# Optimization experiments

Measured on AMD Instinct MI355X. Metric: run time of the kernel, lower is better.

## Reference

```python
import jax, jax.numpy as jnp
import numpy as np

EPS = 1e-08
LN_EPS = 1e-05


def _layernorm(x, g, b):
    mu = jnp.mean(x, axis=-1, keepdims=True)
    var = jnp.var(x, axis=-1, keepdims=True)
    return (x - mu) * jax.lax.rsqrt(var + LN_EPS) * g + b


def _prob(x):
    x = jnp.tanh(x) * 0.499 + 0.5
    return jnp.clip(x / (jnp.sum(x, axis=-1, keepdims=True) + EPS), EPS)


def setup_inputs() -> dict:
    key = jax.random.key(0)
    ks = jax.random.split(key, 8)
    B, N, D = 8, 2048, 1024
    H = 4 * D
    s = 0.02
    return {
        'q': jax.random.normal(ks[0], (B, N, D), jnp.float32),
        'k': jax.random.normal(ks[1], (B, N, D), jnp.float32),
        'v': jax.random.normal(ks[2], (B, N, D), jnp.float32),
        'W_diff': jax.random.normal(ks[3], (D, D), jnp.float32) * s,
        'b_diff': jnp.zeros((D,), jnp.float32),
        'ln_g': jnp.ones((D,), jnp.float32),
        'ln_b': jnp.zeros((D,), jnp.float32),
        'W1': jax.random.normal(ks[4], (H, D), jnp.float32) * s,
        'b1': jnp.zeros((H,), jnp.float32),
        'W2': jax.random.normal(ks[5], (D, H), jnp.float32) * s,
        'b2': jnp.zeros((D,), jnp.float32),
    }


def reference(q, k, v, W_diff, b_diff, ln_g, ln_b, W1, b1, W2, b2):
    D = q.shape[-1]
    q_prob = _prob(q)  # [B,N,D]
    k_prob = _prob(k)  # [B,N,D]
    log_ratio = jnp.log(q_prob) - jnp.log(k_prob)  # [B,N,D]
    # sid[b,i,j] = sum_d (q_prob[b,i,d] - k_prob[b,i,d]) * log_ratio[b,j,d]
    sid = jnp.einsum('bnd,bmd->bnm', q_prob - k_prob, log_ratio)
    sid_sim = -sid
    attn = jax.nn.softmax(sid_sim / (D ** 0.5), axis=-1)  # [B,N,N]
    attn_feat = jnp.einsum('bnm,bmd->bnd', attn, v)
    f_diff = (v - attn_feat) @ W_diff.T + b_diff + q
    h = _layernorm(f_diff, ln_g, ln_b)
    mlp = jax.nn.gelu(h @ W1.T + b1, approximate=False) @ W2.T + b2
    out = mlp + f_diff
    return _layernorm(out, ln_g, ln_b)
```

## Files before the change

kernel.cpp:

```cpp
#include <hip/hip_runtime.h>
#include <math.h>

typedef unsigned short u16;
typedef __attribute__((ext_vector_type(4))) unsigned short u16x4;
typedef __attribute__((ext_vector_type(8))) short s16x8;
typedef __attribute__((ext_vector_type(4))) float f32x4;
typedef __attribute__((ext_vector_type(4))) float f4v;

#define DEVI static __device__ __forceinline__

DEVI u16 f2bf(float f) {
  union { float f; unsigned u; } c; c.f = f;
  return (u16)((c.u + 0x7FFFu + ((c.u >> 16) & 1u)) >> 16);
}
DEVI float bf2f(u16 h) {
  union { unsigned u; float f; } c; c.u = ((unsigned)h) << 16;
  return c.f;
}
DEVI unsigned cvt_pk_bf16(float lo, float hi) {
  unsigned r;
  asm("v_cvt_pk_bf16_f32 %0, %1, %2" : "=v"(r) : "v"(lo), "v"(hi));
  return r;
}

DEVI float tanh_fast(float x) {
  float e = __expf(2.0f * x);
  float r = __builtin_amdgcn_rcpf(e + 1.0f);
  return fmaf(-2.0f, r, 1.0f);
}
DEVI float gelu_fast(float x) {
  float x2 = x * x;
  float u = x * fmaf(x2, 0.0356774081f, 0.7978845608f);
  float e = __expf(2.0f * u);
  float r = __builtin_amdgcn_rcpf(e + 1.0f);
  float t = fmaf(-2.0f, r, 1.0f);
  float hx = 0.5f * x;
  return fmaf(hx, t, hx);
}

DEVI void load_lds16(const void* g, void* l) {
  __builtin_amdgcn_global_load_lds(
      (const __attribute__((address_space(1))) void*)g,
      (__attribute__((address_space(3))) void*)l, 16, 0, 0);
}

#define BAR_VM6() asm volatile("s_waitcnt vmcnt(6)\n\ts_barrier" ::: "memory")
#define BAR_VM4() asm volatile("s_waitcnt vmcnt(4)\n\ts_barrier" ::: "memory")
#define BAR_VM2() asm volatile("s_waitcnt vmcnt(2)\n\ts_barrier" ::: "memory")
#define BAR_VM0() asm volatile("s_waitcnt vmcnt(0)\n\ts_barrier" ::: "memory")
#define BAR_PLAIN() asm volatile("s_barrier" ::: "memory")


__global__ __launch_bounds__(256) void cast_bf4_kernel(
    const float* __restrict__ in, u16* __restrict__ out, int n4) {
  int i = blockIdx.x * 256 + threadIdx.x;
  if (i >= n4) return;
  f4v f = ((const f4v*)in)[i];
  u16x4 o;
  o[0] = f2bf(f[0]); o[1] = f2bf(f[1]); o[2] = f2bf(f[2]); o[3] = f2bf(f[3]);
  ((u16x4*)out)[i] = o;
}

__global__ __launch_bounds__(256) void prob_kernel(
    const float* __restrict__ q, const float* __restrict__ k,
    u16* __restrict__ A, u16* __restrict__ Bm) {
  const int D = 1024;
  size_t row = blockIdx.x;
  int t = threadIdx.x;
  f4v qv = ((const f4v*)(q + row * D))[t];
  f4v kv = ((const f4v*)(k + row * D))[t];
  float tq[4], tk[4];
  float sq = 0.f, sk = 0.f;
#pragma unroll
  for (int i = 0; i < 4; i++) {
    tq[i] = tanh_fast(qv[i]) * 0.499f + 0.5f;
    tk[i] = tanh_fast(kv[i]) * 0.499f + 0.5f;
    sq += tq[i]; sk += tk[i];
  }
#pragma unroll
  for (int off = 32; off > 0; off >>= 1) {
    sq += __shfl_xor(sq, off);
    sk += __shfl_xor(sk, off);
  }
  __shared__ float sbq[4], sbk[4];
  int lane = t & 63, w = t >> 6;
  if (lane == 0) { sbq[w] = sq; sbk[w] = sk; }
  __syncthreads();
  sq = sbq[0] + sbq[1] + sbq[2] + sbq[3];
  sk = sbk[0] + sbk[1] + sbk[2] + sbk[3];
  float iq = 1.0f / (sq + 1e-8f), ik = 1.0f / (sk + 1e-8f);
  u16x4 av, bv;
#pragma unroll
  for (int i = 0; i < 4; i++) {
    float qp = fmaxf(tq[i] * iq, 1e-8f);
    float kp = fmaxf(tk[i] * ik, 1e-8f);
    av[i] = f2bf(qp - kp);
    bv[i] = f2bf(__logf(qp) - __logf(kp));
  }
  ((u16x4*)(A + row * D))[t] = av;
  ((u16x4*)(Bm + row * D))[t] = bv;
}

__global__ __launch_bounds__(256) void transpose_v_kernel(
    const float* __restrict__ v, u16* __restrict__ Vt) {
  const int N = 2048, D = 1024;
  __shared__ float tile[32][33];
  int b = blockIdx.z;
  int d0 = blockIdx.x * 32, n0 = blockIdx.y * 32;
  int tx = threadIdx.x & 31, ty = threadIdx.x >> 5;
  const float* vb = v + (size_t)b * N * D;
  u16* vtb = Vt + (size_t)b * N * D;
#pragma unroll
  for (int i = 0; i < 4; i++)
    tile[ty + i * 8][tx] = vb[(size_t)(n0 + ty + i * 8) * D + d0 + tx];
  __syncthreads();
#pragma unroll
  for (int i = 0; i < 4; i++)
    vtb[(size_t)(d0 + ty + i * 8) * N + n0 + tx] = f2bf(tile[tx][ty + i * 8]);
}

__global__ __launch_bounds__(256) void softmax_rows_kernel(u16* __restrict__ S) {
  const int NN = 2048;
  size_t row = blockIdx.x;
  u16* r = S + row * NN;
  int t = threadIdx.x;
  s16x8 vv = ((const s16x8*)r)[t];
  float x[8];
  float mx = -1e30f;
#pragma unroll
  for (int i = 0; i < 8; i++) { x[i] = bf2f((u16)vv[i]); mx = fmaxf(mx, x[i]); }
#pragma unroll
  for (int off = 32; off > 0; off >>= 1) mx = fmaxf(mx, __shfl_xor(mx, off));
  __shared__ float sm[4], ss[4];
  int lane = t & 63, w = t >> 6;
  if (lane == 0) sm[w] = mx;
  __syncthreads();
  mx = fmaxf(fmaxf(sm[0], sm[1]), fmaxf(sm[2], sm[3]));
  float sum = 0.f;
#pragma unroll
  for (int i = 0; i < 8; i++) { x[i] = __expf(x[i] - mx); sum += x[i]; }
#pragma unroll
  for (int off = 32; off > 0; off >>= 1) sum += __shfl_xor(sum, off);
  if (lane == 0) ss[w] = sum;
  __syncthreads();
  float inv = 1.0f / (ss[0] + ss[1] + ss[2] + ss[3]);
  s16x8 ov;
#pragma unroll
  for (int i = 0; i < 8; i++) ov[i] = (short)f2bf(x[i] * inv);
  ((s16x8*)r)[t] = ov;
}

template <int OUT_BF16>
__global__ __launch_bounds__(256) void layernorm_rows_kernel(
    const float* __restrict__ in, void* __restrict__ outp,
    const float* __restrict__ g, const float* __restrict__ bia) {
  const int D = 1024;
  size_t row = blockIdx.x;
  int t = threadIdx.x;
  f4v xv = ((const f4v*)(in + row * D))[t];
  float s = xv[0] + xv[1] + xv[2] + xv[3];
  float s2 = xv[0] * xv[0] + xv[1] * xv[1] + xv[2] * xv[2] + xv[3] * xv[3];
#pragma unroll
  for (int off = 32; off > 0; off >>= 1) {
    s += __shfl_xor(s, off);
    s2 += __shfl_xor(s2, off);
  }
  __shared__ float sa[4], sb[4];
  int lane = t & 63, w = t >> 6;
  if (lane == 0) { sa[w] = s; sb[w] = s2; }
  __syncthreads();
  s = sa[0] + sa[1] + sa[2] + sa[3];
  s2 = sb[0] + sb[1] + sb[2] + sb[3];
  float mean = s * (1.0f / D);
  float var = s2 * (1.0f / D) - mean * mean;
  float rs = rsqrtf(var + 1e-5f);
  f4v gv = ((const f4v*)g)[t];
  f4v bv = ((const f4v*)bia)[t];
  float y[4];
#pragma unroll
  for (int i = 0; i < 4; i++) y[i] = (xv[i] - mean) * rs * gv[i] + bv[i];
  if (OUT_BF16) {
    u16x4 o; o[0] = f2bf(y[0]); o[1] = f2bf(y[1]); o[2] = f2bf(y[2]); o[3] = f2bf(y[3]);
    ((u16x4*)outp)[row * (D / 4) + t] = o;
  } else {
    f4v o; o[0] = y[0]; o[1] = y[1]; o[2] = y[2]; o[3] = y[3];
    ((f4v*)outp)[row * (D / 4) + t] = o;
  }
}

template <int EPI>
__global__ __launch_bounds__(512, 2) void gemm8_kernel(
    const u16* __restrict__ Ab, const u16* __restrict__ Bb,
    void* __restrict__ Cout,
    const float* __restrict__ aux1, const float* __restrict__ aux2,
    int M, int Nc, int K,
    long sA, long sB, long sC, long sAux1, float scale) {
  __shared__ u16 lds[65536];

  int nwg = gridDim.x;
  int orig = blockIdx.x;
  int swz = (orig & 7) * (nwg >> 3) + (orig >> 3);
  int gxm = M >> 8, gyn = Nc >> 8;
  int pb = gxm * gyn;
  int bz = swz / pb;
  int rem = swz - bz * pb;
  int gsz = gyn << 3;
  int gid = rem / gsz;
  int lr = rem - gid * gsz;
  int bx = (gid << 3) + (lr & 7);
  int by = lr >> 3;
  int m0 = bx << 8, n0 = by << 8;

  const u16* Ap = Ab + (size_t)bz * sA;
  const u16* Bp = Bb + (size_t)bz * sB;

  int t = threadIdx.x, wid = t >> 6, l = t & 63;
  int wr = wid >> 2, wc = wid & 3;
  int sr = l >> 3;
  int scb = ((l & 7) ^ sr) * 8;
  int frow = l & 15, fq = l >> 4, fx = l & 7;

  auto stA = [&](int tile, int h) {
    int slot = tile & 1;
    const u16* g = Ap + (size_t)(m0 + h * 128 + wid * 16 + sr) * K + tile * 64 + scb;
    u16* lb = &lds[slot * 16384 + h * 8192 + wid * 1024];
    load_lds16(g, lb);
    load_lds16(g + (size_t)8 * K, lb + 512);
  };
  auto stB = [&](int tile, int h) {
    int slot = tile & 1;
    const u16* g = Bp + (size_t)(n0 + h * 128 + wid * 16 + sr) * K + tile * 64 + scb;
    u16* lb = &lds[32768 + slot * 16384 + h * 8192 + wid * 1024];
    load_lds16(g, lb);
    load_lds16(g + (size_t)8 * K, lb + 512);
  };

  s16x8 af[4][2], bf[2][2];
  auto rdA = [&](int slot, int h) {
    const u16* base = &lds[slot * 16384 + h * 8192];
#pragma unroll
    for (int m = 0; m < 4; m++) {
      int row = wr * 64 + m * 16 + frow;
#pragma unroll
      for (int kk = 0; kk < 2; kk++) {
        int ch = (kk * 4 + fq) ^ fx;
        af[m][kk] = *(const s16x8*)&base[row * 64 + ch * 8];
      }
    }
  };
  auto rdB = [&](int slot, int h) {
    const u16* base = &lds[32768 + slot * 16384 + h * 8192];
#pragma unroll
    for (int n = 0; n < 2; n++) {
      int row = wc * 32 + n * 16 + frow;
#pragma unroll
      for (int kk = 0; kk < 2; kk++) {
        int ch = (kk * 4 + fq) ^ fx;
        bf[n][kk] = *(const s16x8*)&base[row * 64 + ch * 8];
      }
    }
  };

  f32x4 acc[2][2][4][2];
#pragma unroll
  for (int a = 0; a < 2; a++)
#pragma unroll
    for (int b = 0; b < 2; b++)
#pragma unroll
      for (int m = 0; m < 4; m++)
#pragma unroll
        for (int n = 0; n < 2; n++) acc[a][b][m][n] = (f32x4){0.f, 0.f, 0.f, 0.f};

#define MFMA_Q(QM, QN)                                                        \
  do {                                                                        \
    __builtin_amdgcn_s_setprio(1);                                            \
    _Pragma("unroll") for (int m = 0; m < 4; m++)                             \
        _Pragma("unroll") for (int n = 0; n < 2; n++)                         \
        _Pragma("unroll") for (int kk = 0; kk < 2; kk++)                      \
            acc[QM][QN][m][n] = __builtin_amdgcn_mfma_f32_16x16x32_bf16(      \
                af[m][kk], bf[n][kk], acc[QM][QN][m][n], 0, 0, 0);            \
    __builtin_amdgcn_s_setprio(0);                                            \
  } while (0)

  stA(0, 0); stB(0, 1); stB(0, 0); stA(0, 1); stA(1, 0); stB(1, 1);
  BAR_VM4();

  int nt = K >> 6, niter = nt >> 1;
  for (int i = 0; i < niter - 1; i++) {
    int t0 = 2 * i;
    rdA(0, 0); rdB(0, 0);
    stB(t0 + 1, 0);
    BAR_VM6(); MFMA_Q(0, 0); BAR_PLAIN();
    rdB(0, 1);
    stA(t0 + 1, 1);
    BAR_VM6(); MFMA_Q(0, 1); BAR_PLAIN();
    rdA(0, 1);
    stA(t0 + 2, 0);
    BAR_VM6(); MFMA_Q(1, 1); BAR_PLAIN();
    rdB(0, 0);
    stB(t0 + 2, 1);
    BAR_VM6(); MFMA_Q(1, 0); BAR_PLAIN();
    rdA(1, 0); rdB(1, 0);
    stB(t0 + 2, 0);
    BAR_VM6(); MFMA_Q(0, 0); BAR_PLAIN();
    rdB(1, 1);
    stA(t0 + 2, 1);
    BAR_VM6(); MFMA_Q(0, 1); BAR_PLAIN();
    rdA(1, 1);
    stA(t0 + 3, 0);
    BAR_VM6(); MFMA_Q(1, 1); BAR_PLAIN();
    rdB(1, 0);
    stB(t0 + 3, 1);
    BAR_VM6(); MFMA_Q(1, 0); BAR_PLAIN();
  }
  {
    int t0 = nt - 2;
    rdA(0, 0); rdB(0, 0);
    stB(t0 + 1, 0);
    BAR_VM6(); MFMA_Q(0, 0); BAR_PLAIN();
    rdB(0, 1);
    stA(t0 + 1, 1);
    BAR_VM6(); MFMA_Q(0, 1); BAR_PLAIN();
    rdA(0, 1);
    BAR_VM4(); MFMA_Q(1, 1); BAR_PLAIN();
    rdB(0, 0);
    BAR_VM2(); MFMA_Q(1, 0); BAR_PLAIN();
    rdA(1, 0); rdB(1, 0);
    BAR_VM2(); MFMA_Q(0, 0); BAR_PLAIN();
    rdB(1, 1);
    BAR_VM0(); MFMA_Q(0, 1); BAR_PLAIN();
    rdA(1, 1);
    BAR_PLAIN(); MFMA_Q(1, 1); BAR_PLAIN();
    rdB(1, 0);
    BAR_PLAIN(); MFMA_Q(1, 0);
  }
#undef MFMA_Q

#pragma unroll
  for (int qm = 0; qm < 2; qm++) {
#pragma unroll
    for (int qn = 0; qn < 2; qn++) {
#pragma unroll
      for (int m = 0; m < 4; m++) {
#pragma unroll
        for (int n = 0; n < 2; n++) {
          f32x4 a4 = acc[qm][qn][m][n];
          int gcol = n0 + qn * 128 + wc * 32 + n * 16 + frow;
#pragma unroll
          for (int rp = 0; rp < 2; rp++) {
            int grow0 = m0 + qm * 128 + wr * 64 + m * 16 + fq * 4 + rp * 2;
            size_t ci0 = (size_t)grow0 * Nc + gcol;
            if (EPI == 0) {
              unsigned pk = cvt_pk_bf16(a4[rp * 2] * scale, a4[rp * 2 + 1] * scale);
              ((u16*)Cout)[(size_t)bz * sC + ci0] = (u16)pk;
              ((u16*)Cout)[(size_t)bz * sC + ci0 + Nc] = (u16)(pk >> 16);
            } else if (EPI == 1) {
              float v0 = aux1[(size_t)bz * sAux1 + ci0];
              float v1 = aux1[(size_t)bz * sAux1 + ci0 + Nc];
              unsigned pk = cvt_pk_bf16(v0 - a4[rp * 2], v1 - a4[rp * 2 + 1]);
              ((u16*)Cout)[(size_t)bz * sC + ci0] = (u16)pk;
              ((u16*)Cout)[(size_t)bz * sC + ci0 + Nc] = (u16)(pk >> 16);
            } else if (EPI == 2) {
              float b2v = aux2[gcol];
              ((float*)Cout)[ci0] = a4[rp * 2] + b2v + aux1[ci0];
              ((float*)Cout)[ci0 + Nc] = a4[rp * 2 + 1] + b2v + aux1[ci0 + Nc];
            } else {
              float b2v = aux2[gcol];
              unsigned pk = cvt_pk_bf16(gelu_fast(a4[rp * 2] + b2v),
                                        gelu_fast(a4[rp * 2 + 1] + b2v));
              ((u16*)Cout)[ci0] = (u16)pk;
              ((u16*)Cout)[ci0 + Nc] = (u16)(pk >> 16);
            }
          }
        }
      }
    }
  }
}


extern "C" void kernel_launch(void* const* d_in, const int* in_sizes, int n_in,
                              void* d_out, int out_size, void* d_ws, size_t ws_size,
                              hipStream_t stream) {
  const float* q      = (const float*)d_in[0];
  const float* k      = (const float*)d_in[1];
  const float* v      = (const float*)d_in[2];
  const float* W_diff = (const float*)d_in[3];
  const float* b_diff = (const float*)d_in[4];
  const float* ln_g   = (const float*)d_in[5];
  const float* ln_b   = (const float*)d_in[6];
  const float* W1     = (const float*)d_in[7];
  const float* b1     = (const float*)d_in[8];
  const float* W2     = (const float*)d_in[9];
  const float* b2     = (const float*)d_in[10];

  const int B = 8, N = 2048, D = 1024, H = 4096;
  char* ws = (char*)d_ws;
  u16* A   = (u16*)(ws + 0);
  u16* Bm  = (u16*)(ws + 33554432);
  u16* X   = (u16*)(ws + 33554432);
  u16* Vt  = (u16*)(ws + 67108864);
  u16* S   = (u16*)(ws + 100663296);
  u16* Hbf = (u16*)(ws + 134217728);
  u16* Wd  = (u16*)(ws + 167772160);
  u16* W1b = (u16*)(ws + 169869312);
  u16* W2b = (u16*)(ws + 178257920);
  u16* G   = (u16*)(ws + 0);
  float* out = (float*)d_out;

  cast_bf4_kernel<<<(D * D / 4) / 256, 256, 0, stream>>>(W_diff, Wd, D * D / 4);
  cast_bf4_kernel<<<(H * D / 4) / 256, 256, 0, stream>>>(W1, W1b, H * D / 4);
  cast_bf4_kernel<<<(D * H / 4) / 256, 256, 0, stream>>>(W2, W2b, D * H / 4);

  prob_kernel<<<B * N, 256, 0, stream>>>(q, k, A, Bm);
  transpose_v_kernel<<<dim3(D / 32, N / 32, B), 256, 0, stream>>>(v, Vt);

  gemm8_kernel<0><<<8 * 8 * 8, 512, 0, stream>>>(
      A, Bm, S, nullptr, nullptr, N, N, D,
      (long)N * D, (long)N * D, (long)N * N, 0, -0.03125f);

  softmax_rows_kernel<<<B * N, 256, 0, stream>>>(S);

  gemm8_kernel<1><<<8 * 4 * 8, 512, 0, stream>>>(
      S, Vt, X, v, nullptr, N, D, N,
      (long)N * N, (long)D * N, (long)N * D, (long)N * D, 1.0f);

  gemm8_kernel<2><<<64 * 4, 512, 0, stream>>>(
      X, Wd, out, q, b_diff, B * N, D, D, 0, 0, 0, 0, 1.0f);

  layernorm_rows_kernel<1><<<B * N, 256, 0, stream>>>(out, Hbf, ln_g, ln_b);

  gemm8_kernel<3><<<64 * 16, 512, 0, stream>>>(
      Hbf, W1b, G, nullptr, b1, B * N, H, D, 0, 0, 0, 0, 1.0f);

  gemm8_kernel<2><<<64 * 4, 512, 0, stream>>>(
      G, W2b, out, out, b2, B * N, D, H, 0, 0, 0, 0, 1.0f);

  layernorm_rows_kernel<0><<<B * N, 256, 0, stream>>>(out, out, ln_g, ln_b);
}
```

Baseline: 590.2 us.

## Merge weight casts, store pre-LN output as bf16, double-buffer B fragments

Replaces the three weight-cast launches with one combined cast kernel. The last GEMM now writes the residual sum (mlp + f_diff) as bf16 into scratch, and the final layernorm reads it as bf16, which cuts fp32 write and read traffic. In the GEMM mainloop, B fragments are held in two register sets so two of the four LDS re-reads per half-iteration are dropped, at the cost of more VGPRs. Rounding the pre-layernorm output to bf16 reduces precision of the final result.

After: 578.6 us. Within noise of the previous version (-2.0%).

```diff
diff --git a/kernel.cpp b/kernel.cpp
--- a/kernel.cpp
+++ b/kernel.cpp
@@ -51,14 +51,20 @@
 #define BAR_PLAIN() asm volatile("s_barrier" ::: "memory")
 
 
-__global__ __launch_bounds__(256) void cast_bf4_kernel(
-    const float* __restrict__ in, u16* __restrict__ out, int n4) {
+__global__ __launch_bounds__(256) void cast3_kernel(
+    const float* __restrict__ wd, const float* __restrict__ w1,
+    const float* __restrict__ w2, u16* __restrict__ owd,
+    u16* __restrict__ ow1, u16* __restrict__ ow2) {
+  const int n1 = 262144, n2 = 1048576;
   int i = blockIdx.x * 256 + threadIdx.x;
-  if (i >= n4) return;
-  f4v f = ((const f4v*)in)[i];
+  const float* src; u16* dst; int j;
+  if (i < n1) { src = wd; dst = owd; j = i; }
+  else if (i < n1 + n2) { src = w1; dst = ow1; j = i - n1; }
+  else { src = w2; dst = ow2; j = i - n1 - n2; }
+  f4v f = ((const f4v*)src)[j];
   u16x4 o;
   o[0] = f2bf(f[0]); o[1] = f2bf(f[1]); o[2] = f2bf(f[2]); o[3] = f2bf(f[3]);
-  ((u16x4*)out)[i] = o;
+  ((u16x4*)dst)[j] = o;
 }
 
 __global__ __launch_bounds__(256) void prob_kernel(
@@ -150,14 +156,20 @@
   ((s16x8*)r)[t] = ov;
 }
 
-template <int OUT_BF16>
+template <int IN_BF16, int OUT_BF16>
 __global__ __launch_bounds__(256) void layernorm_rows_kernel(
-    const float* __restrict__ in, void* __restrict__ outp,
+    const void* __restrict__ inp, void* __restrict__ outp,
     const float* __restrict__ g, const float* __restrict__ bia) {
   const int D = 1024;
   size_t row = blockIdx.x;
   int t = threadIdx.x;
-  f4v xv = ((const f4v*)(in + row * D))[t];
+  f4v xv;
+  if (IN_BF16) {
+    u16x4 h4 = ((const u16x4*)inp)[row * (D / 4) + t];
+    xv[0] = bf2f(h4[0]); xv[1] = bf2f(h4[1]); xv[2] = bf2f(h4[2]); xv[3] = bf2f(h4[3]);
+  } else {
+    xv = ((const f4v*)inp)[row * (D / 4) + t];
+  }
   float s = xv[0] + xv[1] + xv[2] + xv[3];
   float s2 = xv[0] * xv[0] + xv[1] * xv[1] + xv[2] * xv[2] + xv[3] * xv[3];
 #pragma unroll
@@ -235,7 +247,7 @@
     load_lds16(g + (size_t)8 * K, lb + 512);
   };
 
-  s16x8 af[4][2], bf[2][2];
+  s16x8 af[4][2], bf0[2][2], bf1[2][2];
   auto rdA = [&](int slot, int h) {
     const u16* base = &lds[slot * 16384 + h * 8192];
 #pragma unroll
@@ -248,7 +260,7 @@
       }
     }
   };
-  auto rdB = [&](int slot, int h) {
+  auto rdB = [&](int slot, int h, s16x8 (&bf)[2][2]) {
     const u16* base = &lds[32768 + slot * 16384 + h * 8192];
 #pragma unroll
     for (int n = 0; n < 2; n++) {
@@ -271,14 +283,14 @@
 #pragma unroll
         for (int n = 0; n < 2; n++) acc[a][b][m][n] = (f32x4){0.f, 0.f, 0.f, 0.f};
 
-#define MFMA_Q(QM, QN)                                                        \
+#define MFMA_Q(QM, QN, BF)                                                    \
   do {                                                                        \
     __builtin_amdgcn_s_setprio(1);                                            \
     _Pragma("unroll") for (int m = 0; m < 4; m++)                             \
         _Pragma("unroll") for (int n = 0; n < 2; n++)                         \
         _Pragma("unroll") for (int kk = 0; kk < 2; kk++)                      \
             acc[QM][QN][m][n] = __builtin_amdgcn_mfma_f32_16x16x32_bf16(      \
-                af[m][kk], bf[n][kk], acc[QM][QN][m][n], 0, 0, 0);            \
+                af[m][kk], BF[n][kk], acc[QM][QN][m][n], 0, 0, 0);            \
     __builtin_amdgcn_s_setprio(0);                                            \
   } while (0)
 
@@ -288,51 +300,47 @@
   int nt = K >> 6, niter = nt >> 1;
   for (int i = 0; i < niter - 1; i++) {
     int t0 = 2 * i;
-    rdA(0, 0); rdB(0, 0);
+    rdA(0, 0); rdB(0, 0, bf0);
     stB(t0 + 1, 0);
-    BAR_VM6(); MFMA_Q(0, 0); BAR_PLAIN();
-    rdB(0, 1);
+    BAR_VM6(); MFMA_Q(0, 0, bf0); BAR_PLAIN();
+    rdB(0, 1, bf1);
     stA(t0 + 1, 1);
-    BAR_VM6(); MFMA_Q(0, 1); BAR_PLAIN();
+    BAR_VM6(); MFMA_Q(0, 1, bf1); BAR_PLAIN();
     rdA(0, 1);
     stA(t0 + 2, 0);
-    BAR_VM6(); MFMA_Q(1, 1); BAR_PLAIN();
-    rdB(0, 0);
+    BAR_VM6(); MFMA_Q(1, 1, bf1); BAR_PLAIN();
     stB(t0 + 2, 1);
-    BAR_VM6(); MFMA_Q(1, 0); BAR_PLAIN();
-    rdA(1, 0); rdB(1, 0);
+    BAR_VM6(); MFMA_Q(1, 0, bf0); BAR_PLAIN();
+    rdA(1, 0); rdB(1, 0, bf0);
     stB(t0 + 2, 0);
-    BAR_VM6(); MFMA_Q(0, 0); BAR_PLAIN();
-    rdB(1, 1);
+    BAR_VM6(); MFMA_Q(0, 0, bf0); BAR_PLAIN();
+    rdB(1, 1, bf1);
     stA(t0 + 2, 1);
-    BAR_VM6(); MFMA_Q(0, 1); BAR_PLAIN();
+    BAR_VM6(); MFMA_Q(0, 1, bf1); BAR_PLAIN();
     rdA(1, 1);
     stA(t0 + 3, 0);
-    BAR_VM6(); MFMA_Q(1, 1); BAR_PLAIN();
-    rdB(1, 0);
+    BAR_VM6(); MFMA_Q(1, 1, bf1); BAR_PLAIN();
     stB(t0 + 3, 1);
-    BAR_VM6(); MFMA_Q(1, 0); BAR_PLAIN();
+    BAR_VM6(); MFMA_Q(1, 0, bf0); BAR_PLAIN();
   }
   {
     int t0 = nt - 2;
-    rdA(0, 0); rdB(0, 0);
+    rdA(0, 0); rdB(0, 0, bf0);
     stB(t0 + 1, 0);
-    BAR_VM6(); MFMA_Q(0, 0); BAR_PLAIN();
-    rdB(0, 1);
+    BAR_VM6(); MFMA_Q(0, 0, bf0); BAR_PLAIN();
+    rdB(0, 1, bf1);
     stA(t0 + 1, 1);
-    BAR_VM6(); MFMA_Q(0, 1); BAR_PLAIN();
+    BAR_VM6(); MFMA_Q(0, 1, bf1); BAR_PLAIN();
     rdA(0, 1);
-    BAR_VM4(); MFMA_Q(1, 1); BAR_PLAIN();
-    rdB(0, 0);
-    BAR_VM2(); MFMA_Q(1, 0); BAR_PLAIN();
-    rdA(1, 0); rdB(1, 0);
-    BAR_VM2(); MFMA_Q(0, 0); BAR_PLAIN();
-    rdB(1, 1);
-    BAR_VM0(); MFMA_Q(0, 1); BAR_PLAIN();
+    BAR_VM4(); MFMA_Q(1, 1, bf1); BAR_PLAIN();
+    BAR_VM2(); MFMA_Q(1, 0, bf0); BAR_PLAIN();
+    rdA(1, 0); rdB(1, 0, bf0);
+    BAR_VM2(); MFMA_Q(0, 0, bf0); BAR_PLAIN();
+    rdB(1, 1, bf1);
+    BAR_VM0(); MFMA_Q(0, 1, bf1); BAR_PLAIN();
     rdA(1, 1);
-    BAR_PLAIN(); MFMA_Q(1, 1); BAR_PLAIN();
-    rdB(1, 0);
-    BAR_PLAIN(); MFMA_Q(1, 0);
+    BAR_PLAIN(); MFMA_Q(1, 1, bf1); BAR_PLAIN();
+    BAR_PLAIN(); MFMA_Q(1, 0, bf0);
   }
 #undef MFMA_Q
 
@@ -364,10 +372,16 @@
               float b2v = aux2[gcol];
               ((float*)Cout)[ci0] = a4[rp * 2] + b2v + aux1[ci0];
               ((float*)Cout)[ci0 + Nc] = a4[rp * 2 + 1] + b2v + aux1[ci0 + Nc];
-            } else {
+            } else if (EPI == 3) {
               float b2v = aux2[gcol];
               unsigned pk = cvt_pk_bf16(gelu_fast(a4[rp * 2] + b2v),
                                         gelu_fast(a4[rp * 2 + 1] + b2v));
+              ((u16*)Cout)[ci0] = (u16)pk;
+              ((u16*)Cout)[ci0 + Nc] = (u16)(pk >> 16);
+            } else {
+              float b2v = aux2[gcol];
+              unsigned pk = cvt_pk_bf16(a4[rp * 2] + b2v + aux1[ci0],
+                                        a4[rp * 2 + 1] + b2v + aux1[ci0 + Nc]);
               ((u16*)Cout)[ci0] = (u16)pk;
               ((u16*)Cout)[ci0 + Nc] = (u16)(pk >> 16);
             }
@@ -396,21 +410,19 @@
 
   const int B = 8, N = 2048, D = 1024, H = 4096;
   char* ws = (char*)d_ws;
-  u16* A   = (u16*)(ws + 0);
-  u16* Bm  = (u16*)(ws + 33554432);
-  u16* X   = (u16*)(ws + 33554432);
-  u16* Vt  = (u16*)(ws + 67108864);
-  u16* S   = (u16*)(ws + 100663296);
-  u16* Hbf = (u16*)(ws + 134217728);
-  u16* Wd  = (u16*)(ws + 167772160);
-  u16* W1b = (u16*)(ws + 169869312);
-  u16* W2b = (u16*)(ws + 178257920);
-  u16* G   = (u16*)(ws + 0);
+  u16* A    = (u16*)(ws + 0);
+  u16* Bm   = (u16*)(ws + 33554432);
+  u16* X    = (u16*)(ws + 33554432);
+  u16* Vt   = (u16*)(ws + 67108864);
+  u16* S    = (u16*)(ws + 100663296);
+  u16* Hbf  = (u16*)(ws + 134217728);
+  u16* Wd   = (u16*)(ws + 167772160);
+  u16* W1b  = (u16*)(ws + 169869312);
+  u16* W2b  = (u16*)(ws + 178257920);
+  u16* G    = (u16*)(ws + 0);
   float* out = (float*)d_out;
 
-  cast_bf4_kernel<<<(D * D / 4) / 256, 256, 0, stream>>>(W_diff, Wd, D * D / 4);
-  cast_bf4_kernel<<<(H * D / 4) / 256, 256, 0, stream>>>(W1, W1b, H * D / 4);
-  cast_bf4_kernel<<<(D * H / 4) / 256, 256, 0, stream>>>(W2, W2b, D * H / 4);
+  cast3_kernel<<<9216, 256, 0, stream>>>(W_diff, W1, W2, Wd, W1b, W2b);
 
   prob_kernel<<<B * N, 256, 0, stream>>>(q, k, A, Bm);
   transpose_v_kernel<<<dim3(D / 32, N / 32, B), 256, 0, stream>>>(v, Vt);
@@ -428,13 +440,13 @@
   gemm8_kernel<2><<<64 * 4, 512, 0, stream>>>(
       X, Wd, out, q, b_diff, B * N, D, D, 0, 0, 0, 0, 1.0f);
 
-  layernorm_rows_kernel<1><<<B * N, 256, 0, stream>>>(out, Hbf, ln_g, ln_b);
+  layernorm_rows_kernel<0, 1><<<B * N, 256, 0, stream>>>(out, Hbf, ln_g, ln_b);
 
   gemm8_kernel<3><<<64 * 16, 512, 0, stream>>>(
       Hbf, W1b, G, nullptr, b1, B * N, H, D, 0, 0, 0, 0, 1.0f);
 
-  gemm8_kernel<2><<<64 * 4, 512, 0, stream>>>(
-      G, W2b, out, out, b2, B * N, D, H, 0, 0, 0, 0, 1.0f);
-
-  layernorm_rows_kernel<0><<<B * N, 256, 0, stream>>>(out, out, ln_g, ln_b);
-}
+  gemm8_kernel<5><<<64 * 4, 512, 0, stream>>>(
+      G, W2b, Hbf, out, b2, B * N, D, H, 0, 0, 0, 0, 1.0f);
+
+  layernorm_rows_kernel<1, 0><<<B * N, 256, 0, stream>>>(Hbf, out, ln_g, ln_b);
+}
```
